# Kernel tuning notes

Hardware: AMD Instinct MI355X
Metric: run time of the kernel (lower is better)

Reference implementation:

```python
import jax, jax.numpy as jnp
import numpy as np

QDEPTH = 8
WIDTH = 64
HEIGHT = 64
WIRES = 12  # ceil(log2(64*64))
BATCH = 1024


def setup_inputs() -> dict:
    key = jax.random.key(0)
    k1, k2 = jax.random.split(key)
    x = jax.random.normal(k1, (BATCH, 1, WIDTH, HEIGHT), dtype=jnp.float32)
    # torch.nn.Parameter(torch.randn(weight_shape) * 0.4)
    weights = jax.random.normal(k2, (QDEPTH, WIRES, 3), dtype=jnp.float32) * 0.4
    return {"x": x, "weights": weights, "reps": 1}


def _rot_matrices(angles):
    # angles: (L, W, 3) -> (L, W, 2, 2) complex64; Rot(phi, theta, omega) = RZ(omega) RY(theta) RZ(phi)
    phi, theta, omega = angles[..., 0], angles[..., 1], angles[..., 2]
    c = jnp.cos(theta * 0.5).astype(jnp.complex64)
    s = jnp.sin(theta * 0.5).astype(jnp.complex64)
    ep = jnp.exp(-0.5j * (phi + omega).astype(jnp.complex64))  # e^{-i(phi+omega)/2}
    em = jnp.exp(-0.5j * (phi - omega).astype(jnp.complex64))  # e^{-i(phi-omega)/2}
    row0 = jnp.stack([ep * c, -jnp.conj(em) * s], axis=-1)
    row1 = jnp.stack([em * s, jnp.conj(ep) * c], axis=-1)
    return jnp.stack([row0, row1], axis=-2)


def _apply_1q(state, U, wire):
    # state: (B, 2, 2, ..., 2); apply 2x2 U on axis wire+1
    ax = wire + 1
    s = jnp.moveaxis(state, ax, -1)
    s = s @ U.T  # out[..., i] = sum_j U[i, j] s[..., j]
    return jnp.moveaxis(s, -1, ax)


def _apply_cnot(state, control, target):
    c, t = control + 1, target + 1
    s0, s1 = jnp.split(state, 2, axis=c)   # control = 0 / 1 halves
    s1 = jnp.flip(s1, axis=t)              # X on target where control = 1
    return jnp.concatenate([s0, s1], axis=c)


def _sel_layer(state, mats_l, r):
    # one StronglyEntanglingLayers layer: Rot on every wire, then CNOT ring of range r
    for w in range(WIRES):
        state = _apply_1q(state, mats_l[w], w)
    for w in range(WIRES):
        state = _apply_cnot(state, w, (w + r) % WIRES)
    return state


def _circuit(state, weights, reps):
    mats = _rot_matrices(jnp.tanh(weights))  # qw_map.tanh applied to raw weights
    for _ in range(reps):
        for l in range(QDEPTH):
            r = (l % (WIRES - 1)) + 1  # PennyLane default ranges
            layer = jax.checkpoint(lambda s, m, _r=r: _sel_layer(s, m, _r))
            state = layer(state, mats[l])
    return state


def reference(x, weights, reps):
    b = x.shape[0]
    v = x.reshape(b, -1)  # (b, 4096)
    norm = jnp.linalg.norm(v, axis=-1, keepdims=True)
    v = (v / norm).astype(jnp.complex64)
    state = v.reshape((b,) + (2,) * WIRES)
    state = _circuit(state, weights, reps)
    out = state.reshape(b, -1) * norm
    return out.reshape(b, 1, WIDTH, HEIGHT)
```

## Files before the change

### kernel.cpp

```cpp
#include <hip/hip_runtime.h>

#define WIRES   12
#define NSTATE  4096
#define QDEPTH  8
#define BLOCK   256
#define PER_T   16

using f2 = __attribute__((ext_vector_type(2))) float;

__device__ __forceinline__ int slotf(int a) { return a + (a >> 4); }

constexpr int colF(int l, int j) {
    int rr = (l % (WIRES - 1)) + 1;
    int v = 1 << j;
    for (int k = WIRES - 1; k >= 0; --k) {
        int bc = 11 - k;
        int bt = 11 - ((k + rr) % WIRES);
        v ^= ((v >> bc) & 1) << bt;
    }
    return v;
}
struct ColsT { int v[QDEPTH][WIRES]; };
constexpr ColsT mkCols() {
    ColsT c{};
    for (int l = 0; l < QDEPTH; ++l)
        for (int j = 0; j < WIRES; ++j) c.v[l][j] = colF(l, j);
    return c;
}
static __device__ const ColsT COLS = mkCols();

#define OFF_KP 288
#define OFF_KW 544
#define OFF_AN 800

__global__ void setup_kernel(const float* __restrict__ wts, f2* __restrict__ mg)
{
    const int t = threadIdx.x;
    if (t < QDEPTH * WIRES) {
        float th = tanhf(wts[t * 3 + 1]);
        float c = cosf(0.5f * th), s = sinf(0.5f * th);
        mg[(t / 12) * 36 + (t % 12) * 3 + 0] = f2{ c,  c};
        mg[(t / 12) * 36 + (t % 12) * 3 + 1] = f2{-s, -s};
        mg[(t / 12) * 36 + (t % 12) * 3 + 2] = f2{ s,  s};
    }
    if (t < 64) {
        int l = t >> 3, j = t & 7;
        float aP = 0.5f * tanhf(wts[(l * 12 + (7  - j)) * 3 + 0]);
        float aW = 0.5f * tanhf(wts[(l * 12 + (11 - j)) * 3 + 2]);
        mg[OFF_AN + l * 8 + j] = f2{aP, aW};
    }
    {
        int l = t >> 5, k = (t >> 1) & 15;
        bool isW = (t & 1) != 0;
        float ph = 0.f;
        #pragma unroll
        for (int j = 0; j < 4; ++j) {
            int wire  = isW ? (3 - j) : (11 - j);
            int comp  = isW ? 2 : 0;
            float a   = 0.5f * tanhf(wts[(l * 12 + wire) * 3 + comp]);
            ph += ((k >> j) & 1) ? a : -a;
        }
        float s, c;
        sincosf(ph, &s, &c);
        int base = isW ? OFF_KW : OFF_KP;
        mg[base + l * 32 + k * 2 + 0] = f2{ c, c};
        mg[base + l * 32 + k * 2 + 1] = f2{-s, s};
    }
}

template<int P>
__device__ __forceinline__ void gateR(f2 r[PER_T], f2 cc, f2 ms, f2 ss)
{
    #pragma unroll
    for (int pr = 0; pr < PER_T / 2; pr += 2) {
        const int k0 = ((pr >> P) << (P + 1)) | (pr & ((1 << P) - 1));
        const int k1 = k0 | (1 << P);
        const int q  = pr + 1;
        const int j0 = ((q >> P) << (P + 1)) | (q & ((1 << P) - 1));
        const int j1 = j0 | (1 << P);
        f2 a0, b0, a1, b1;
        asm("v_pk_mul_f32 %0, %4, %8\n\t"
            "v_pk_mul_f32 %1, %4, %10\n\t"
            "v_pk_mul_f32 %2, %6, %8\n\t"
            "v_pk_mul_f32 %3, %6, %10\n\t"
            "v_pk_fma_f32 %0, %5, %9, %0\n\t"
            "v_pk_fma_f32 %1, %5, %8, %1\n\t"
            "v_pk_fma_f32 %2, %7, %9, %2\n\t"
            "v_pk_fma_f32 %3, %7, %8, %3"
            : "=&v"(a0), "=&v"(b0), "=&v"(a1), "=&v"(b1)
            : "v"(r[k0]), "v"(r[k1]), "v"(r[j0]), "v"(r[j1]),
              "v"(cc), "v"(ms), "v"(ss));
        r[k0] = a0; r[k1] = b0; r[j0] = a1; r[j1] = b1;
    }
}

__device__ __forceinline__ void dmul2(f2& a0, f2& a1, f2 d0r, f2 d0w,
                                      f2 d1r, f2 d1w)
{
    f2 o0, o1;
    asm("v_pk_mul_f32 %0, %2, %4\n\t"
        "v_pk_mul_f32 %1, %3, %6\n\t"
        "v_pk_fma_f32 %0, %2, %5, %0 op_sel:[1,0,0] op_sel_hi:[0,1,1]\n\t"
        "v_pk_fma_f32 %1, %3, %7, %1 op_sel:[1,0,0] op_sel_hi:[0,1,1]"
        : "=&v"(o0), "=&v"(o1)
        : "v"(a0), "v"(a1), "v"(d0r), "v"(d0w), "v"(d1r), "v"(d1w));
    a0 = o0; a1 = o1;
}

__device__ __forceinline__ void diag(f2 r[PER_T], const f2* __restrict__ AN,
                                     const f2* __restrict__ KF, int g, bool isW)
{
    float ph = 0.f;
    #pragma unroll
    for (int j = 0; j < 8; ++j) {
        float a = isW ? AN[j].y : AN[j].x;
        ph += ((g >> j) & 1) ? a : -a;
    }
    float s, c;
    sincosf(ph, &s, &c);
    const f2 Lr = f2{c, c}, Lw = f2{-s, s};
    #pragma unroll
    for (int k = 0; k < PER_T; k += 2)
        dmul2(r[k], r[k + 1], Lr, Lw, Lr, Lw);
    #pragma unroll
    for (int k = 0; k < PER_T; k += 2)
        dmul2(r[k], r[k + 1], KF[2*k], KF[2*k + 1], KF[2*k + 2], KF[2*k + 3]);
}

__global__ __launch_bounds__(BLOCK, 4) void qsim_kernel(
    const float* __restrict__ x,
    const f2*    __restrict__ mg,
    const int*   __restrict__ reps_ptr,
    float*       __restrict__ out,
    int write_mode)
{
    __shared__ f2 st[4352];

    const int g   = threadIdx.x;
    const int b   = blockIdx.x;
    const int ghi = g >> 4, glo = g & 15;
    const int w1b = 17 * g;
    const int rb1 = 272 * ghi + glo;
    const int rb2 = 17 * ghi + glo;

    const float4* xb4 = (const float4*)(x + (size_t)b * NSTATE) + g * 4;
    f2 r[PER_T];
    #pragma unroll
    for (int c = 0; c < 4; ++c) {
        float4 v = xb4[c];
        r[4*c+0] = f2{v.x, 0.f};
        r[4*c+1] = f2{v.y, 0.f};
        r[4*c+2] = f2{v.z, 0.f};
        r[4*c+3] = f2{v.w, 0.f};
    }

    const int reps = reps_ptr[0];
    for (int rep = 0; rep < reps; ++rep) {
        #pragma unroll 1
        for (int l = 0; l < QDEPTH; ++l) {
            const f2* CS = mg + l * 36;
            const f2* KP = mg + OFF_KP + l * 32;
            const f2* KW = mg + OFF_KW + l * 32;
            const f2* AN = mg + OFF_AN + l * 8;

            diag(r, AN, KP, g, false);

            gateR<3>(r, CS[8*3],  CS[8*3+1],  CS[8*3+2]);
            gateR<2>(r, CS[9*3],  CS[9*3+1],  CS[9*3+2]);
            gateR<1>(r, CS[10*3], CS[10*3+1], CS[10*3+2]);
            gateR<0>(r, CS[11*3], CS[11*3+1], CS[11*3+2]);

            #pragma unroll
            for (int k = 0; k < PER_T; ++k) st[w1b + k] = r[k];
            __syncthreads();
            #pragma unroll
            for (int k = 0; k < PER_T; ++k) r[k] = st[rb1 + 17 * k];

            gateR<3>(r, CS[4*3], CS[4*3+1], CS[4*3+2]);
            gateR<2>(r, CS[5*3], CS[5*3+1], CS[5*3+2]);
            gateR<1>(r, CS[6*3], CS[6*3+1], CS[6*3+2]);
            gateR<0>(r, CS[7*3], CS[7*3+1], CS[7*3+2]);

            #pragma unroll
            for (int k = 0; k < PER_T; ++k) st[rb1 + 17 * k] = r[k];
            __syncthreads();
            #pragma unroll
            for (int k = 0; k < PER_T; ++k) r[k] = st[rb2 + 272 * k];

            gateR<3>(r, CS[0*3], CS[0*3+1], CS[0*3+2]);
            gateR<2>(r, CS[1*3], CS[1*3+1], CS[1*3+2]);
            gateR<1>(r, CS[2*3], CS[2*3+1], CS[2*3+2]);
            gateR<0>(r, CS[3*3], CS[3*3+1], CS[3*3+2]);

            diag(r, AN, KW, g, true);

            #pragma unroll
            for (int k = 0; k < PER_T; ++k) st[rb2 + 272 * k] = r[k];
            __syncthreads();

            {
                int Fg = 0;
                #pragma unroll
                for (int j = 0; j < 8; ++j)
                    Fg ^= ((g >> j) & 1) ? COLS.v[l][4 + j] : 0;
                const int c0 = COLS.v[l][0], c1 = COLS.v[l][1];
                const int c2 = COLS.v[l][2], c3 = COLS.v[l][3];
                #pragma unroll
                for (int k = 0; k < PER_T; ++k) {
                    int ck = ((k & 1) ? c0 : 0) ^ ((k & 2) ? c1 : 0) ^
                             ((k & 4) ? c2 : 0) ^ ((k & 8) ? c3 : 0);
                    r[k] = st[slotf(Fg ^ ck)];
                }
            }
            __syncthreads();
        }
    }

    if (write_mode == 0) {
        float4* ob4 = (float4*)(out + (size_t)b * NSTATE) + g * 4;
        #pragma unroll
        for (int c = 0; c < 4; ++c)
            ob4[c] = make_float4(r[4*c].x, r[4*c+1].x, r[4*c+2].x, r[4*c+3].x);
    } else {
        float4* ob4 = (float4*)((float2*)out + (size_t)b * NSTATE) + g * 8;
        #pragma unroll
        for (int k = 0; k < PER_T; k += 2)
            ob4[k >> 1] = make_float4(r[k].x, r[k].y, r[k+1].x, r[k+1].y);
    }
}

extern "C" void kernel_launch(void* const* d_in, const int* in_sizes, int n_in,
                              void* d_out, int out_size, void* d_ws, size_t ws_size,
                              hipStream_t stream) {
    const float* x    = (const float*)d_in[0];
    const float* wts  = (const float*)d_in[1];
    const int*   reps = (const int*)d_in[2];
    float*       out  = (float*)d_out;
    f2*          mg   = (f2*)d_ws;
    (void)in_sizes; (void)n_in; (void)ws_size;

    const int write_mode = (out_size >= 2 * 1024 * NSTATE) ? 1 : 0;

    setup_kernel<<<1, 256, 0, stream>>>(wts, mg);
    qsim_kernel<<<1024, BLOCK, 0, stream>>>(x, mg, reps, out, write_mode);
}
```

Baseline: 134.9 us.

## Use DPP cross-lane gates and swizzled LDS layout to cut one shared-memory transpose

Restructures each layer so two of the qubit wires are handled across adjacent lanes via DPP quad permutes instead of in-register pairs. This lets the 12 wires be covered with only two shared-memory exchanges plus the CNOT permutation gather, removing one full LDS write/read/barrier round per layer. The LDS layout switches to an XOR-swizzled, unpadded layout with 16-byte vector reads/writes, and the CNOT column table is remapped into the swizzled index space. The diagonal phase tables are reassigned to match the new wire-to-position mapping. It adds DPP instructions and more complex index math, and correctness depends on the swizzle and wire remapping being consistent.

```diff
diff --git a/kernel.cpp b/kernel.cpp
--- a/kernel.cpp
+++ b/kernel.cpp
@@ -7,8 +7,6 @@
 #define PER_T   16
 
 using f2 = __attribute__((ext_vector_type(2))) float;
-
-__device__ __forceinline__ int slotf(int a) { return a + (a >> 4); }
 
 constexpr int colF(int l, int j) {
     int rr = (l % (WIRES - 1)) + 1;
@@ -20,14 +18,19 @@
     }
     return v;
 }
-struct ColsT { int v[QDEPTH][WIRES]; };
-constexpr ColsT mkCols() {
-    ColsT c{};
+
+constexpr int sigma_c(int x) {
+    int p = ((x >> 6) & 15) | (((x >> 10) & 3) << 4) | ((x & 63) << 6);
+    return p ^ (((p >> 4) & 7) << 1);
+}
+struct SColsT { int v[QDEPTH][WIRES]; };
+constexpr SColsT mkSCols() {
+    SColsT c{};
     for (int l = 0; l < QDEPTH; ++l)
-        for (int j = 0; j < WIRES; ++j) c.v[l][j] = colF(l, j);
+        for (int j = 0; j < WIRES; ++j) c.v[l][j] = sigma_c(colF(l, j));
     return c;
 }
-static __device__ const ColsT COLS = mkCols();
+static __device__ const SColsT SCOLS = mkSCols();
 
 #define OFF_KP 288
 #define OFF_KW 544
@@ -45,8 +48,9 @@
     }
     if (t < 64) {
         int l = t >> 3, j = t & 7;
-        float aP = 0.5f * tanhf(wts[(l * 12 + (7  - j)) * 3 + 0]);
-        float aW = 0.5f * tanhf(wts[(l * 12 + (11 - j)) * 3 + 2]);
+        float aP = 0.5f * tanhf(wts[(l * 12 + (7 - j)) * 3 + 0]);
+        int wj = (j == 0) ? 1 : (j == 1) ? 0 : (13 - j);
+        float aW = 0.5f * tanhf(wts[(l * 12 + wj) * 3 + 2]);
         mg[OFF_AN + l * 8 + j] = f2{aP, aW};
     }
     {
@@ -55,9 +59,9 @@
         float ph = 0.f;
         #pragma unroll
         for (int j = 0; j < 4; ++j) {
-            int wire  = isW ? (3 - j) : (11 - j);
-            int comp  = isW ? 2 : 0;
-            float a   = 0.5f * tanhf(wts[(l * 12 + wire) * 3 + comp]);
+            int wire = isW ? (5 - j) : (11 - j);
+            int comp = isW ? 2 : 0;
+            float a  = 0.5f * tanhf(wts[(l * 12 + wire) * 3 + comp]);
             ph += ((k >> j) & 1) ? a : -a;
         }
         float s, c;
@@ -94,6 +98,42 @@
     }
 }
 
+template<int CTRL>
+__device__ __forceinline__ f2 dpp_xor(f2 v) {
+    f2 o;
+    o.x = __int_as_float(__builtin_amdgcn_update_dpp(
+            0, __float_as_int(v.x), CTRL, 0xF, 0xF, true));
+    o.y = __int_as_float(__builtin_amdgcn_update_dpp(
+            0, __float_as_int(v.y), CTRL, 0xF, 0xF, true));
+    return o;
+}
+
+template<int CTRL>
+__device__ __forceinline__ void dgateR(f2 r[PER_T], f2 cc, f2 k2)
+{
+    #pragma unroll
+    for (int k0 = 0; k0 < PER_T; k0 += 4) {
+        f2 p0 = dpp_xor<CTRL>(r[k0 + 0]);
+        f2 p1 = dpp_xor<CTRL>(r[k0 + 1]);
+        f2 p2 = dpp_xor<CTRL>(r[k0 + 2]);
+        f2 p3 = dpp_xor<CTRL>(r[k0 + 3]);
+        f2 o0, o1, o2, o3;
+        asm("v_pk_mul_f32 %0, %4, %12\n\t"
+            "v_pk_mul_f32 %1, %5, %12\n\t"
+            "v_pk_mul_f32 %2, %6, %12\n\t"
+            "v_pk_mul_f32 %3, %7, %12\n\t"
+            "v_pk_fma_f32 %0, %8, %13, %0\n\t"
+            "v_pk_fma_f32 %1, %9, %13, %1\n\t"
+            "v_pk_fma_f32 %2, %10, %13, %2\n\t"
+            "v_pk_fma_f32 %3, %11, %13, %3"
+            : "=&v"(o0), "=&v"(o1), "=&v"(o2), "=&v"(o3)
+            : "v"(r[k0]), "v"(r[k0+1]), "v"(r[k0+2]), "v"(r[k0+3]),
+              "v"(p0), "v"(p1), "v"(p2), "v"(p3),
+              "v"(cc), "v"(k2));
+        r[k0] = o0; r[k0+1] = o1; r[k0+2] = o2; r[k0+3] = o3;
+    }
+}
+
 __device__ __forceinline__ void dmul2(f2& a0, f2& a1, f2 d0r, f2 d0w,
                                       f2 d1r, f2 d1w)
 {
@@ -134,14 +174,19 @@
     float*       __restrict__ out,
     int write_mode)
 {
-    __shared__ f2 st[4352];
-
-    const int g   = threadIdx.x;
-    const int b   = blockIdx.x;
-    const int ghi = g >> 4, glo = g & 15;
-    const int w1b = 17 * g;
-    const int rb1 = 272 * ghi + glo;
-    const int rb2 = 17 * ghi + glo;
+    __shared__ alignas(16) f2 st[4096];
+    float4* const stv = (float4*)st;
+
+    const int g = threadIdx.x;
+    const int b = blockIdx.x;
+    const bool hb0 = (g & 1) != 0;
+    const bool hb1 = (g & 2) != 0;
+
+    const int Pg  = ((g >> 2) & 15) | (((g >> 6) & 3) << 4) | ((g & 3) << 10);
+    const int B0W = Pg ^ (((g >> 6) & 3) << 1);
+    const int B1W = B0W ^ 8;
+    const int baseR4 = ((g & 3) << 3) | ((g >> 2) << 5);
+    const int hj     = g & 7;
 
     const float4* xb4 = (const float4*)(x + (size_t)b * NSTATE) + g * 4;
     f2 r[PER_T];
@@ -165,51 +210,52 @@
 
             diag(r, AN, KP, g, false);
 
+            gateR<0>(r, CS[11*3], CS[11*3+1], CS[11*3+2]);
+            gateR<1>(r, CS[10*3], CS[10*3+1], CS[10*3+2]);
+            gateR<2>(r, CS[9*3],  CS[9*3+1],  CS[9*3+2]);
             gateR<3>(r, CS[8*3],  CS[8*3+1],  CS[8*3+2]);
-            gateR<2>(r, CS[9*3],  CS[9*3+1],  CS[9*3+2]);
-            gateR<1>(r, CS[10*3], CS[10*3+1], CS[10*3+2]);
-            gateR<0>(r, CS[11*3], CS[11*3+1], CS[11*3+2]);
+            dgateR<0xB1>(r, CS[7*3], hb0 ? CS[7*3+2] : CS[7*3+1]);
+            dgateR<0x4E>(r, CS[6*3], hb1 ? CS[6*3+2] : CS[6*3+1]);
 
             #pragma unroll
-            for (int k = 0; k < PER_T; ++k) st[w1b + k] = r[k];
+            for (int k = 0; k < PER_T; ++k)
+                st[((k & 1) ? B1W : B0W) + (k << 6)] = r[k];
             __syncthreads();
+
             #pragma unroll
-            for (int k = 0; k < PER_T; ++k) r[k] = st[rb1 + 17 * k];
-
-            gateR<3>(r, CS[4*3], CS[4*3+1], CS[4*3+2]);
-            gateR<2>(r, CS[5*3], CS[5*3+1], CS[5*3+2]);
-            gateR<1>(r, CS[6*3], CS[6*3+1], CS[6*3+2]);
-            gateR<0>(r, CS[7*3], CS[7*3+1], CS[7*3+2]);
+            for (int j = 0; j < 8; ++j) {
+                float4 v = stv[baseR4 | (j ^ hj)];
+                r[2*j]     = f2{v.x, v.y};
+                r[2*j + 1] = f2{v.z, v.w};
+            }
+
+            gateR<0>(r, CS[5*3], CS[5*3+1], CS[5*3+2]);
+            gateR<1>(r, CS[4*3], CS[4*3+1], CS[4*3+2]);
+            gateR<2>(r, CS[3*3], CS[3*3+1], CS[3*3+2]);
+            gateR<3>(r, CS[2*3], CS[2*3+1], CS[2*3+2]);
+            dgateR<0xB1>(r, CS[1*3], hb0 ? CS[1*3+2] : CS[1*3+1]);
+            dgateR<0x4E>(r, CS[0*3], hb1 ? CS[0*3+2] : CS[0*3+1]);
+
+            diag(r, AN, KW, g, true);
 
             #pragma unroll
-            for (int k = 0; k < PER_T; ++k) st[rb1 + 17 * k] = r[k];
+            for (int j = 0; j < 8; ++j)
+                stv[baseR4 | (j ^ hj)] =
+                    make_float4(r[2*j].x, r[2*j].y, r[2*j+1].x, r[2*j+1].y);
             __syncthreads();
-            #pragma unroll
-            for (int k = 0; k < PER_T; ++k) r[k] = st[rb2 + 272 * k];
-
-            gateR<3>(r, CS[0*3], CS[0*3+1], CS[0*3+2]);
-            gateR<2>(r, CS[1*3], CS[1*3+1], CS[1*3+2]);
-            gateR<1>(r, CS[2*3], CS[2*3+1], CS[2*3+2]);
-            gateR<0>(r, CS[3*3], CS[3*3+1], CS[3*3+2]);
-
-            diag(r, AN, KW, g, true);
-
-            #pragma unroll
-            for (int k = 0; k < PER_T; ++k) st[rb2 + 272 * k] = r[k];
-            __syncthreads();
 
             {
-                int Fg = 0;
+                int Sg = 0;
                 #pragma unroll
                 for (int j = 0; j < 8; ++j)
-                    Fg ^= ((g >> j) & 1) ? COLS.v[l][4 + j] : 0;
-                const int c0 = COLS.v[l][0], c1 = COLS.v[l][1];
-                const int c2 = COLS.v[l][2], c3 = COLS.v[l][3];
+                    Sg ^= ((g >> j) & 1) ? SCOLS.v[l][4 + j] : 0;
+                const int s0 = SCOLS.v[l][0], s1 = SCOLS.v[l][1];
+                const int s2 = SCOLS.v[l][2], s3 = SCOLS.v[l][3];
                 #pragma unroll
                 for (int k = 0; k < PER_T; ++k) {
-                    int ck = ((k & 1) ? c0 : 0) ^ ((k & 2) ? c1 : 0) ^
-                             ((k & 4) ? c2 : 0) ^ ((k & 8) ? c3 : 0);
-                    r[k] = st[slotf(Fg ^ ck)];
+                    int sck = ((k & 1) ? s0 : 0) ^ ((k & 2) ? s1 : 0) ^
+                              ((k & 4) ? s2 : 0) ^ ((k & 8) ? s3 : 0);
+                    r[k] = st[Sg ^ sck];
                 }
             }
             __syncthreads();
```

Result: slower. 138.5 us (+2.7%).
